# Optimization experiments

Measured on AMD Instinct MI355X. Metric: run time of the kernel, lower is better.

Reference implementation:

```python
import jax, jax.numpy as jnp
import numpy as np

B, S, T, H, NH, NL = 16, 128, 64, 128, 8, 4
DH = H // NH
FF = 2 * H
SCALE = 1.0 / float(np.sqrt(DH))


def _ln(x, s, b):
    m = x.mean(-1, keepdims=True)
    v = ((x - m) ** 2).mean(-1, keepdims=True)
    return (x - m) * jax.lax.rsqrt(v + 1e-5) * s + b


def _block(x, mask, p):
    Wq, bq, Wk, bk, Wv, bv, Wo, bo, s1, c1, W1, d1, W2, d2, s2, c2 = p
    N, L, _ = x.shape
    q = (x @ Wq + bq).reshape(N, L, NH, DH)
    k = (x @ Wk + bk).reshape(N, L, NH, DH)
    v = (x @ Wv + bv).reshape(N, L, NH, DH)
    scores = jnp.einsum('nqhd,nkhd->nhqk', q, k) * SCALE
    scores = jnp.where(mask[:, None, :, :], scores, -1e9)
    a = jax.nn.softmax(scores, axis=-1)
    o = jnp.einsum('nhqk,nkhd->nqhd', a, v).reshape(N, L, H)
    x = _ln(x + o @ Wo + bo, s1, c1)
    h = jax.nn.relu(x @ W1 + d1)
    return _ln(x + h @ W2 + d2, s2, c2)


def setup_inputs():
    key = jax.random.key(0)
    ks = jax.random.split(key, 16)
    g = lambda k, shape: jax.random.normal(k, shape, jnp.float32) * 0.02
    return {
        'polylines': jax.random.normal(ks[0], (B, S, T, H), jnp.float32),
        'lengths': jax.random.randint(ks[1], (B, S), 0, T + 1),
        'proj_w': g(ks[2], (H, H)), 'proj_b': jnp.zeros((H,), jnp.float32),
        'proj_ln_s': jnp.ones((H,), jnp.float32), 'proj_ln_b': jnp.zeros((H,), jnp.float32),
        'pos_emb': g(ks[3], (1, T, H)),
        'Wq': g(ks[4], (NL, H, H)), 'bq': jnp.zeros((NL, H), jnp.float32),
        'Wk': g(ks[5], (NL, H, H)), 'bk': jnp.zeros((NL, H), jnp.float32),
        'Wv': g(ks[6], (NL, H, H)), 'bv': jnp.zeros((NL, H), jnp.float32),
        'Wo': g(ks[7], (NL, H, H)), 'bo': jnp.zeros((NL, H), jnp.float32),
        'ln1_s': jnp.ones((NL, H), jnp.float32), 'ln1_b': jnp.zeros((NL, H), jnp.float32),
        'W1': g(ks[8], (NL, H, FF)), 'b1': jnp.zeros((NL, FF), jnp.float32),
        'W2': g(ks[9], (NL, FF, H)), 'b2': jnp.zeros((NL, H), jnp.float32),
        'ln2_s': jnp.ones((NL, H), jnp.float32), 'ln2_b': jnp.zeros((NL, H), jnp.float32),
    }


def reference(polylines, lengths, proj_w, proj_b, proj_ln_s, proj_ln_b, pos_emb,
              Wq, bq, Wk, bk, Wv, bv, Wo, bo, ln1_s, ln1_b, W1, b1, W2, b2, ln2_s, ln2_b):
    # valid[b,s,t] = t < lengths[b,s]; lengths==0 -> polyline absent (fully padded)
    valid = jnp.arange(T)[None, None, :] < lengths[:, :, None]  # [B,S,T]
    x = jnp.where(valid[..., None], polylines, -1.0)            # -1 pad as in np.pad(constant_values=-1)
    # mask_temporal[b,s] = outer(valid[b,s], valid[b,s])
    mask_t = (valid[:, :, :, None] & valid[:, :, None, :]).reshape(B * S, T, T)
    # mask_spatial[b,t] = outer(valid[b,:,t], valid[b,:,t])
    vs = jnp.transpose(valid, (0, 2, 1))                        # [B,T,S]
    mask_s = (vs[:, :, :, None] & vs[:, :, None, :]).reshape(B * T, S, S)

    x = x.reshape(B * S, T, H)
    x = jax.nn.relu(_ln(x @ proj_w + proj_b, proj_ln_s, proj_ln_b))  # MLP: Linear->LN->ReLU
    x = x + pos_emb[:, :T, :]

    mask = mask_t
    for i in range(NL):
        if i == NL // 2:
            # switch from temporal to spatial attention: [B*S,T,H] -> [B*T,S,H]
            x = x.reshape(B, S, T, H).transpose(0, 2, 1, 3).reshape(B * T, S, H)
            mask = mask_s
        p = (Wq[i], bq[i], Wk[i], bk[i], Wv[i], bv[i], Wo[i], bo[i],
             ln1_s[i], ln1_b[i], W1[i], b1[i], W2[i], b2[i], ln2_s[i], ln2_b[i])
        x = _block(x, mask, p)
    # faithful to original final reshape (treats [B*T,S,H] buffer as [B,S,T,H])
    return x.reshape(B, S, T, H)[:, 0, :]
```

## Files before the change

### kernel.cpp

```cpp
#include <hip/hip_runtime.h>

typedef short short8 __attribute__((ext_vector_type(8)));
typedef short short4_t __attribute__((ext_vector_type(4)));
typedef float floatx4 __attribute__((ext_vector_type(4)));
typedef unsigned short ushort_t;

#define B_ 16
#define S_ 128
#define T_ 64
#define H_ 128
#define FF_ 256
#define SCALEQK 0.25f

#define OFFP 0
#define OFFQ(l) (16384 + (l) * 65536)
#define OFFK(l) (OFFQ(l) + 16384)
#define OFFV(l) (OFFQ(l) + 32768)
#define OFFO(l) (OFFQ(l) + 49152)
#define OFFW1(l) (278528 + (l) * 65536)
#define OFFW2(l) (OFFW1(l) + 32768)

__device__ __forceinline__ float b2f(ushort_t u) {
    union { unsigned int i; float f; } x; x.i = ((unsigned int)u) << 16; return x.f;
}
__device__ __forceinline__ ushort_t f2b(float f) {
    union { float f; unsigned int i; } x; x.f = f;
    unsigned int r = x.i + 0x7fffu + ((x.i >> 16) & 1u);
    return (ushort_t)(r >> 16);
}
__device__ __forceinline__ int pack2b(float a, float b) {
    return (int)f2b(a) | ((int)f2b(b) << 16);
}

struct WtEnt { const float* src; int N; int K; int nclog2; int dstoff; };
struct WtArgs { WtEnt e[25]; };

__global__ __launch_bounds__(256) void wt_kernel(WtArgs a, ushort_t* __restrict__ dst) {
    WtEnt ent = a.e[blockIdx.x];
    const int tiles_c = ent.N >> 5;
    const int nt = (ent.K >> 5) * tiles_c;
    const int t = blockIdx.y;
    if (t >= nt) return;
    const int tc = t & (tiles_c - 1);
    const int tr = t >> ent.nclog2;
    __shared__ float ld[32 * 33];
    const int tid = threadIdx.x;
#pragma unroll
    for (int i = 0; i < 4; ++i) {
        int e = tid + i * 256;
        int rr = e >> 5, cc = e & 31;
        ld[rr * 33 + cc] = ent.src[(tr * 32 + rr) * ent.N + tc * 32 + cc];
    }
    __syncthreads();
    ushort_t* d = dst + ent.dstoff;
#pragma unroll
    for (int i = 0; i < 4; ++i) {
        int e = tid + i * 256;
        int rr = e >> 5, cc = e & 31;
        d[(tc * 32 + rr) * ent.K + tr * 32 + cc] = f2b(ld[cc * 33 + rr]);
    }
}

template<int RT, int CT, int KK>
__device__ __forceinline__ void mm_g(const ushort_t* aL, int sa,
                                     const ushort_t* __restrict__ wT,
                                     int colbase, int lane, floatx4 (&acc)[RT][CT]) {
    const int l15 = lane & 15, lq8 = (lane >> 4) * 8;
#pragma unroll
    for (int r = 0; r < RT; ++r)
#pragma unroll
        for (int c = 0; c < CT; ++c) acc[r][c] = (floatx4){0.f, 0.f, 0.f, 0.f};
#pragma unroll
    for (int k0 = 0; k0 < KK; k0 += 32) {
        short8 b[CT];
#pragma unroll
        for (int c = 0; c < CT; ++c)
            b[c] = *(const short8*)&wT[(colbase + c * 16 + l15) * KK + k0 + lq8];
#pragma unroll
        for (int r = 0; r < RT; ++r) {
            short8 a = *(const short8*)&aL[(r * 16 + l15) * sa + k0 + lq8];
#pragma unroll
            for (int c = 0; c < CT; ++c)
                acc[r][c] = __builtin_amdgcn_mfma_f32_16x16x32_bf16(a, b[c], acc[r][c], 0, 0, 0);
        }
    }
}

template<int RT, int CT>
__device__ __forceinline__ void add_bias(floatx4 (&acc)[RT][CT], const float* b,
                                         int colbase, int l15) {
#pragma unroll
    for (int c = 0; c < CT; ++c) {
        float bc = b[colbase + c * 16 + l15];
#pragma unroll
        for (int r = 0; r < RT; ++r)
#pragma unroll
            for (int g = 0; g < 4; ++g) acc[r][c][g] += bc;
    }
}

template<int RT, int CT>
__device__ __forceinline__ void add_resid_reg(floatx4 (&acc)[RT][CT],
                                              const float (&res)[RT][CT][4]) {
#pragma unroll
    for (int r = 0; r < RT; ++r)
#pragma unroll
        for (int c = 0; c < CT; ++c)
#pragma unroll
            for (int g = 0; g < 4; ++g) acc[r][c][g] += res[r][c][g];
}
template<int RT, int CT>
__device__ __forceinline__ void save_resid(float (&res)[RT][CT][4],
                                           const floatx4 (&acc)[RT][CT]) {
#pragma unroll
    for (int r = 0; r < RT; ++r)
#pragma unroll
        for (int c = 0; c < CT; ++c)
#pragma unroll
            for (int g = 0; g < 4; ++g) res[r][c][g] = acc[r][c][g];
}

template<int RT, int CT>
__device__ __forceinline__ void st_n(const floatx4 (&acc)[RT][CT], ushort_t* dst, int stride,
                                     int colbase, int l15, int lq) {
#pragma unroll
    for (int r = 0; r < RT; ++r)
#pragma unroll
        for (int g = 0; g < 4; ++g) {
            int row = r * 16 + lq * 4 + g;
#pragma unroll
            for (int c = 0; c < CT; ++c)
                dst[row * stride + colbase + c * 16 + l15] = f2b(acc[r][c][g]);
        }
}

template<int RT, int CT>
__device__ __forceinline__ void st_t(const floatx4 (&acc)[RT][CT], ushort_t* dst, int stride,
                                     int colbase, int l15, int lq) {
#pragma unroll
    for (int r = 0; r < RT; ++r)
#pragma unroll
        for (int c = 0; c < CT; ++c) {
            int d = colbase + c * 16 + l15;
            short4_t p;
#pragma unroll
            for (int g = 0; g < 4; ++g) p[g] = (short)f2b(acc[r][c][g]);
            *(short4_t*)&dst[d * stride + r * 16 + lq * 4] = p;
        }
}

template<int RT, int CT>
__device__ __forceinline__ void ln_norm(floatx4 (&acc)[RT][CT], float* redL,
                                        const float* lns, const float* lnb,
                                        int colbase, int l15, int lq, int wv) {
#pragma unroll
    for (int r = 0; r < RT; ++r)
#pragma unroll
        for (int g = 0; g < 4; ++g) {
            float s = 0.f, q = 0.f;
#pragma unroll
            for (int c = 0; c < CT; ++c) { float v = acc[r][c][g]; s += v; q += v * v; }
            s += __shfl_xor(s, 1); s += __shfl_xor(s, 2); s += __shfl_xor(s, 4); s += __shfl_xor(s, 8);
            q += __shfl_xor(q, 1); q += __shfl_xor(q, 2); q += __shfl_xor(q, 4); q += __shfl_xor(q, 8);
            if (l15 == 0) {
                int row = r * 16 + lq * 4 + g;
                redL[row * 8 + wv] = s;
                redL[row * 8 + 4 + wv] = q;
            }
        }
    __syncthreads();
#pragma unroll
    for (int r = 0; r < RT; ++r)
#pragma unroll
        for (int g = 0; g < 4; ++g) {
            int row = r * 16 + lq * 4 + g;
            float4 S = *(float4*)&redL[row * 8];
            float4 Q = *(float4*)&redL[row * 8 + 4];
            float mean = (S.x + S.y + S.z + S.w) * (1.f / 128.f);
            float var = (Q.x + Q.y + Q.z + Q.w) * (1.f / 128.f) - mean * mean;
            float rstd = rsqrtf(var + 1e-5f);
#pragma unroll
            for (int c = 0; c < CT; ++c) {
                int col = colbase + c * 16 + l15;
                acc[r][c][g] = (acc[r][c][g] - mean) * rstd * lns[col] + lnb[col];
            }
        }
}

template<int JT>
__device__ __forceinline__ void softmax_pack(floatx4 (&st)[JT], bool iv, unsigned jm,
                                             int (&px)[JT][2]) {
    float ev[JT][4];
    float mx = -3.0e38f;
#pragma unroll
    for (int jt = 0; jt < JT; ++jt)
#pragma unroll
        for (int g = 0; g < 4; ++g) {
            bool ok = iv && ((jm >> (jt * 4 + g)) & 1u);
            float s = ok ? st[jt][g] * SCALEQK : -1e9f;
            ev[jt][g] = s; mx = fmaxf(mx, s);
        }
    mx = fmaxf(mx, __shfl_xor(mx, 16)); mx = fmaxf(mx, __shfl_xor(mx, 32));
    float sum = 0.f;
#pragma unroll
    for (int jt = 0; jt < JT; ++jt)
#pragma unroll
        for (int g = 0; g < 4; ++g) { float e = __expf(ev[jt][g] - mx); ev[jt][g] = e; sum += e; }
    sum += __shfl_xor(sum, 16); sum += __shfl_xor(sum, 32);
    float inv = 1.f / sum;
#pragma unroll
    for (int jt = 0; jt < JT; ++jt) {
        px[jt][0] = pack2b(ev[jt][0] * inv, ev[jt][1] * inv);
        px[jt][1] = pack2b(ev[jt][2] * inv, ev[jt][3] * inv);
    }
}

__device__ __forceinline__ short8 pfrag(const int (*px)[2], int jc, int lq, int l15) {
    const int jA = (lq & 1) * 32 + l15;
    int a0 = __shfl(px[jc * 2][0], jA);
    int a1 = __shfl(px[jc * 2][1], jA);
    int a2 = __shfl(px[jc * 2][0], jA + 16);
    int a3 = __shfl(px[jc * 2][1], jA + 16);
    int b0 = __shfl(px[jc * 2 + 1][0], jA);
    int b1 = __shfl(px[jc * 2 + 1][1], jA);
    int b2 = __shfl(px[jc * 2 + 1][0], jA + 16);
    int b3 = __shfl(px[jc * 2 + 1][1], jA + 16);
    const bool t = (lq >> 1) != 0;
    union { int4 i; short8 s; } u;
    u.i = make_int4(t ? b0 : a0, t ? b1 : a1, t ? b2 : a2, t ? b3 : a3);
    return u.s;
}
__device__ __forceinline__ short8 vfrag(const ushort_t* vT, int stride, int row, int off) {
    int2 a = *(const int2*)&vT[row * stride + off];
    int2 b = *(const int2*)&vT[row * stride + off + 4];
    union { int4 i; short8 s; } u;
    u.i = make_int4(a.x, a.y, b.x, b.y);
    return u.s;
}

__global__ __launch_bounds__(256, 2) void k1_mega(
    const float* __restrict__ poly, const int* __restrict__ lens,
    const ushort_t* __restrict__ wt,
    const float* __restrict__ projb, const float* __restrict__ pls,
    const float* __restrict__ plb, const float* __restrict__ pos,
    const float* __restrict__ bq0, const float* __restrict__ bk0,
    const float* __restrict__ bv0, const float* __restrict__ bo0,
    const float* __restrict__ l1s0, const float* __restrict__ l1b0,
    const float* __restrict__ b10, const float* __restrict__ b20,
    const float* __restrict__ l2s0, const float* __restrict__ l2b0,
    const float* __restrict__ bq1, const float* __restrict__ bk1,
    const float* __restrict__ bv1,
    ushort_t* __restrict__ o1, float* __restrict__ xr0f)
{
    __shared__ ushort_t pool[34816];
    __shared__ float redL[512];
    __shared__ float psL[8 * 68];
    __shared__ float q1L[128];
    ushort_t* xL = pool;
    ushort_t* qL = pool + 8704;
    ushort_t* kL = pool + 17408;
    ushort_t* vT = pool + 26112;
    ushort_t* hL = pool + 17408;

    const int tid = threadIdx.x, lane = tid & 63, wv = tid >> 6;
    const int l15 = lane & 15, lq = lane >> 4;
    const int gid = blockIdx.x;
    const int len = lens[gid];

    {
        const float* pg = poly + (size_t)gid * 8192;
#pragma unroll
        for (int it = 0; it < 8; ++it) {
            int e4 = (tid + it * 256) * 4;
            int row = e4 >> 7, col = e4 & 127;
            float4 f = *(const float4*)(pg + e4);
            if (row >= len) { f.x = -1.f; f.y = -1.f; f.z = -1.f; f.w = -1.f; }
            short4_t u;
            u[0] = (short)f2b(f.x); u[1] = (short)f2b(f.y);
            u[2] = (short)f2b(f.z); u[3] = (short)f2b(f.w);
            *(short4_t*)&xL[row * 136 + col] = u;
        }
    }
    __syncthreads();

    floatx4 a2[4][2];
    float xre[4][2][4];

    mm_g<4, 2, 128>(xL, 136, wt + OFFP, wv * 32, lane, a2);
    add_bias<4, 2>(a2, projb, wv * 32, l15);
    ln_norm<4, 2>(a2, redL, pls, plb, wv * 32, l15, lq, wv);
    __syncthreads();
#pragma unroll
    for (int r = 0; r < 4; ++r)
#pragma unroll
        for (int gg = 0; gg < 4; ++gg) {
            int row = r * 16 + lq * 4 + gg;
#pragma unroll
            for (int c = 0; c < 2; ++c) {
                int col = wv * 32 + c * 16 + l15;
                float v = fmaxf(a2[r][c][gg], 0.f) + pos[row * 128 + col];
                xre[r][c][gg] = v;
                xL[row * 136 + col] = f2b(v);
            }
        }
    __syncthreads();

    mm_g<4, 2, 128>(xL, 136, wt + OFFQ(0), wv * 32, lane, a2);
    add_bias<4, 2>(a2, bq0, wv * 32, l15);
    st_n<4, 2>(a2, qL, 136, wv * 32, l15, lq);
    mm_g<4, 2, 128>(xL, 136, wt + OFFK(0), wv * 32, lane, a2);
    add_bias<4, 2>(a2, bk0, wv * 32, l15);
    st_n<4, 2>(a2, kL, 136, wv * 32, l15, lq);
    mm_g<4, 2, 128>(xL, 136, wt + OFFV(0), wv * 32, lane, a2);
    add_bias<4, 2>(a2, bv0, wv * 32, l15);
    st_t<4, 2>(a2, vT, 68, wv * 32, l15, lq);
    __syncthreads();

    {
        const int iRow = wv * 16 + l15;
        const bool iv = iRow < len;
        unsigned jm = 0;
#pragma unroll
        for (int jt = 0; jt < 4; ++jt)
#pragma unroll
            for (int gg = 0; gg < 4; ++gg)
                if (jt * 16 + lq * 4 + gg < len) jm |= (1u << (jt * 4 + gg));
        for (int h = 0; h < 8; ++h) {
            const int hc = h * 16;
            short8 z8 = {0, 0, 0, 0, 0, 0, 0, 0};
            short8 bqf = z8;
            if (lq < 2) bqf = *(const short8*)&qL[iRow * 136 + hc + lq * 8];
            floatx4 st[4];
#pragma unroll
            for (int jt = 0; jt < 4; ++jt) {
                short8 ak = z8;
                if (lq < 2) ak = *(const short8*)&kL[(jt * 16 + l15) * 136 + hc + lq * 8];
                floatx4 zz = {0.f, 0.f, 0.f, 0.f};
                st[jt] = __builtin_amdgcn_mfma_f32_16x16x32_bf16(ak, bqf, zz, 0, 0, 0);
            }
            int px[4][2];
            softmax_pack<4>(st, iv, jm, px);
            floatx4 ao = {0.f, 0.f, 0.f, 0.f};
#pragma unroll
            for (int jc = 0; jc < 2; ++jc) {
                short8 av = vfrag(vT, 68, hc + l15, jc * 32 + lq * 8);
                short8 bp = pfrag(px, jc, lq, l15);
                ao = __builtin_amdgcn_mfma_f32_16x16x32_bf16(av, bp, ao, 0, 0, 0);
            }
            short4_t w;
#pragma unroll
            for (int gg = 0; gg < 4; ++gg) w[gg] = (short)f2b(ao[gg]);
            *(short4_t*)&qL[iRow * 136 + hc + lq * 4] = w;
        }
    }
    __syncthreads();

    mm_g<4, 2, 128>(qL, 136, wt + OFFO(0), wv * 32, lane, a2);
    add_bias<4, 2>(a2, bo0, wv * 32, l15);
    add_resid_reg<4, 2>(a2, xre);
    ln_norm<4, 2>(a2, redL, l1s0, l1b0, wv * 32, l15, lq, wv);
    save_resid<4, 2>(xre, a2);
    st_n<4, 2>(a2, xL, 136, wv * 32, l15, lq);
    __syncthreads();

    {
        floatx4 a4[4][4];
        mm_g<4, 4, 128>(xL, 136, wt + OFFW1(0), wv * 64, lane, a4);
        add_bias<4, 4>(a4, b10, wv * 64, l15);
#pragma unroll
        for (int r = 0; r < 4; ++r)
#pragma unroll
            for (int c = 0; c < 4; ++c)
#pragma unroll
                for (int gg = 0; gg < 4; ++gg) a4[r][c][gg] = fmaxf(a4[r][c][gg], 0.f);
        st_n<4, 4>(a4, hL, 272, wv * 64, l15, lq);
    }
    __syncthreads();

    mm_g<4, 2, 256>(hL, 272, wt + OFFW2(0), wv * 32, lane, a2);
    add_bias<4, 2>(a2, b20, wv * 32, l15);
    add_resid_reg<4, 2>(a2, xre);
    ln_norm<4, 2>(a2, redL, l2s0, l2b0, wv * 32, l15, lq, wv);
    save_resid<4, 2>(xre, a2);
    st_n<4, 2>(a2, xL, 136, wv * 32, l15, lq);
    if (lq == 0) {
#pragma unroll
        for (int c = 0; c < 2; ++c)
            xr0f[(size_t)gid * 128 + wv * 32 + c * 16 + l15] = a2[0][c][0];
    }
    __syncthreads();

    mm_g<4, 2, 128>(xL, 136, wt + OFFK(1), wv * 32, lane, a2);
    add_bias<4, 2>(a2, bk1, wv * 32, l15);
    st_n<4, 2>(a2, kL, 136, wv * 32, l15, lq);
    mm_g<4, 2, 128>(xL, 136, wt + OFFV(1), wv * 32, lane, a2);
    add_bias<4, 2>(a2, bv1, wv * 32, l15);
    st_t<4, 2>(a2, vT, 68, wv * 32, l15, lq);
    if (tid < 128) {
        int d = tid;
        float a = bq1[d];
        const ushort_t* wq = wt + OFFQ(1) + d * 128;
#pragma unroll 4
        for (int j0 = 0; j0 < 128; j0 += 8) {
            short8 w8 = *(const short8*)&wq[j0];
            short8 x8 = *(const short8*)&xL[j0];
#pragma unroll
            for (int q = 0; q < 8; ++q)
                a = fmaf(b2f((ushort_t)x8[q]), b2f((ushort_t)w8[q]), a);
        }
        q1L[d] = a;
    }
    __syncthreads();

    {
        int h = tid >> 5, jj = tid & 31;
        int hc = h * 16;
        float s[2];
#pragma unroll
        for (int half = 0; half < 2; ++half) {
            int j = jj + half * 32;
            float a = 0.f;
            short8 k0v = *(const short8*)&kL[j * 136 + hc];
            short8 k1v = *(const short8*)&kL[j * 136 + hc + 8];
#pragma unroll
            for (int q = 0; q < 8; ++q) {
                a = fmaf(q1L[hc + q], b2f((ushort_t)k0v[q]), a);
                a = fmaf(q1L[hc + 8 + q], b2f((ushort_t)k1v[q]), a);
            }
            s[half] = (j < len) ? a * SCALEQK : -1e9f;
        }
        float mx = fmaxf(s[0], s[1]);
#pragma unroll
        for (int d = 1; d < 32; d <<= 1) mx = fmaxf(mx, __shfl_xor(mx, d));
        float e0 = __expf(s[0] - mx), e1 = __expf(s[1] - mx);
        float sum = e0 + e1;
#pragma unroll
        for (int d = 1; d < 32; d <<= 1) sum += __shfl_xor(sum, d);
        float inv = 1.f / sum;
        psL[h * 68 + jj] = e0 * inv;
        psL[h * 68 + jj + 32] = e1 * inv;
    }
    __syncthreads();
    if (tid < 128) {
        int h = tid >> 4, d = tid & 15, hc = h * 16;
        float a = 0.f;
#pragma unroll 4
        for (int j0 = 0; j0 < 64; j0 += 4) {
            float4 p4 = *(const float4*)&psL[h * 68 + j0];
            short4_t v4 = *(const short4_t*)&vT[(hc + d) * 68 + j0];
            a += p4.x * b2f((ushort_t)v4[0]) + p4.y * b2f((ushort_t)v4[1])
               + p4.z * b2f((ushort_t)v4[2]) + p4.w * b2f((ushort_t)v4[3]);
        }
        o1[(size_t)gid * 128 + hc + d] = f2b(a);
    }
}

__global__ __launch_bounds__(256, 1) void k2_mega(
    const ushort_t* __restrict__ o1, const float* __restrict__ xr0f,
    const int* __restrict__ lens, const ushort_t* __restrict__ wt,
    const float* __restrict__ bq, const float* __restrict__ bk,
    const float* __restrict__ bv, const float* __restrict__ bo,
    const float* __restrict__ l1s, const float* __restrict__ l1b,
    const float* __restrict__ b1, const float* __restrict__ b2,
    const float* __restrict__ l2s, const float* __restrict__ l2b,
    float* __restrict__ outp)
{
    __shared__ ushort_t pool[69632];
    __shared__ float redL[1024];
    __shared__ int vldL[128];
    ushort_t* xL = pool;
    ushort_t* qL = pool + 17408;
    ushort_t* kL = pool + 34816;
    ushort_t* vT = pool + 52224;
    ushort_t* hL = pool + 34816;

    const int tid = threadIdx.x, lane = tid & 63, wv = tid >> 6;
    const int l15 = lane & 15, lq = lane >> 4;
    const int b = blockIdx.x;
    const size_t rowg = (size_t)b * 128;

#pragma unroll
    for (int it = 0; it < 8; ++it) {
        int e8 = tid + it * 256;
        int row = e8 >> 4, kg = e8 & 15;
        *(short8*)&xL[row * 136 + kg * 8] = *(const short8*)&o1[(rowg + row) * 128 + kg * 8];
    }
    if (tid < 128) vldL[tid] = (lens[b * 128 + tid] > 0) ? 1 : 0;
    __syncthreads();

    unsigned jm = 0;
#pragma unroll
    for (int jt = 0; jt < 8; ++jt)
#pragma unroll
        for (int g = 0; g < 4; ++g)
            if (vldL[jt * 16 + lq * 4 + g]) jm |= (1u << (jt * 4 + g));

    float xre[8][2][4];
#pragma unroll
    for (int r = 0; r < 8; ++r)
#pragma unroll
        for (int c = 0; c < 2; ++c)
#pragma unroll
            for (int g = 0; g < 4; ++g)
                xre[r][c][g] = xr0f[(rowg + r * 16 + lq * 4 + g) * 128 + wv * 32 + c * 16 + l15];

    floatx4 a2[8][2];

    for (int l = 1; l < 4; ++l) {
        if (l >= 2) {
            mm_g<8, 2, 128>(xL, 136, wt + OFFQ(l), wv * 32, lane, a2);
            add_bias<8, 2>(a2, bq + l * H_, wv * 32, l15);
            st_n<8, 2>(a2, qL, 136, wv * 32, l15, lq);
            mm_g<8, 2, 128>(xL, 136, wt + OFFK(l), wv * 32, lane, a2);
            add_bias<8, 2>(a2, bk + l * H_, wv * 32, l15);
            st_n<8, 2>(a2, kL, 136, wv * 32, l15, lq);
            mm_g<8, 2, 128>(xL, 136, wt + OFFV(l), wv * 32, lane, a2);
            add_bias<8, 2>(a2, bv + l * H_, wv * 32, l15);
            st_t<8, 2>(a2, vT, 136, wv * 32, l15, lq);
            __syncthreads();
            for (int h = 0; h < 8; ++h) {
                const int hc = h * 16;
#pragma unroll
                for (int iblk = 0; iblk < 2; ++iblk) {
                    const int iRow = iblk * 64 + wv * 16 + l15;
                    const bool iv = vldL[iRow] != 0;
                    short8 z8 = {0, 0, 0, 0, 0, 0, 0, 0};
                    short8 bqf = z8;
                    if (lq < 2) bqf = *(const short8*)&qL[iRow * 136 + hc + lq * 8];
                    floatx4 st[8];
#pragma unroll
                    for (int jt = 0; jt < 8; ++jt) {
                        short8 ak = z8;
                        if (lq < 2) ak = *(const short8*)&kL[(jt * 16 + l15) * 136 + hc + lq * 8];
                        floatx4 zz = {0.f, 0.f, 0.f, 0.f};
                        st[jt] = __builtin_amdgcn_mfma_f32_16x16x32_bf16(ak, bqf, zz, 0, 0, 0);
                    }
                    int px[8][2];
                    softmax_pack<8>(st, iv, jm, px);
                    floatx4 ao = {0.f, 0.f, 0.f, 0.f};
#pragma unroll
                    for (int jc = 0; jc < 4; ++jc) {
                        short8 av = vfrag(vT, 136, hc + l15, jc * 32 + lq * 8);
                        short8 bp = pfrag(px, jc, lq, l15);
                        ao = __builtin_amdgcn_mfma_f32_16x16x32_bf16(av, bp, ao, 0, 0, 0);
                    }
                    short4_t w;
#pragma unroll
                    for (int g = 0; g < 4; ++g) w[g] = (short)f2b(ao[g]);
                    *(short4_t*)&qL[iRow * 136 + hc + lq * 4] = w;
                }
            }
            __syncthreads();
        }

        const ushort_t* aIn = (l == 1) ? xL : qL;
        mm_g<8, 2, 128>(aIn, 136, wt + OFFO(l), wv * 32, lane, a2);
        add_bias<8, 2>(a2, bo + l * H_, wv * 32, l15);
        add_resid_reg<8, 2>(a2, xre);
        ln_norm<8, 2>(a2, redL, l1s + l * H_, l1b + l * H_, wv * 32, l15, lq, wv);
        save_resid<8, 2>(xre, a2);
        st_n<8, 2>(a2, xL, 136, wv * 32, l15, lq);
        __syncthreads();

        {
            floatx4 a4[8][4];
            mm_g<8, 4, 128>(xL, 136, wt + OFFW1(l), wv * 64, lane, a4);
            add_bias<8, 4>(a4, b1 + l * FF_, wv * 64, l15);
#pragma unroll
            for (int r = 0; r < 8; ++r)
#pragma unroll
                for (int c = 0; c < 4; ++c)
#pragma unroll
                    for (int g = 0; g < 4; ++g) a4[r][c][g] = fmaxf(a4[r][c][g], 0.f);
            st_n<8, 4>(a4, hL, 272, wv * 64, l15, lq);
        }
        __syncthreads();

        mm_g<8, 2, 256>(hL, 272, wt + OFFW2(l), wv * 32, lane, a2);
        add_bias<8, 2>(a2, b2 + l * H_, wv * 32, l15);
        add_resid_reg<8, 2>(a2, xre);
        ln_norm<8, 2>(a2, redL, l2s + l * H_, l2b + l * H_, wv * 32, l15, lq, wv);
        if (l == 3) {
#pragma unroll
            for (int r = 0; r < 4; ++r)
#pragma unroll
                for (int c = 0; c < 2; ++c)
#pragma unroll
                    for (int g = 0; g < 4; ++g) {
                        int row = r * 16 + lq * 4 + g;
                        outp[((size_t)(b * 64 + row)) * 128 + wv * 32 + c * 16 + l15] = a2[r][c][g];
                    }
        } else {
            save_resid<8, 2>(xre, a2);
            st_n<8, 2>(a2, xL, 136, wv * 32, l15, lq);
            __syncthreads();
        }
    }
}

extern "C" void kernel_launch(void* const* d_in, const int* in_sizes, int n_in,
                              void* d_out, int out_size, void* d_ws, size_t ws_size,
                              hipStream_t stream)
{
    const float* poly   = (const float*)d_in[0];
    const int*   lens   = (const int*)d_in[1];
    const float* proj_w = (const float*)d_in[2];
    const float* proj_b = (const float*)d_in[3];
    const float* pls    = (const float*)d_in[4];
    const float* plb    = (const float*)d_in[5];
    const float* pos    = (const float*)d_in[6];
    const float* Wq = (const float*)d_in[7];
    const float* bq = (const float*)d_in[8];
    const float* Wk = (const float*)d_in[9];
    const float* bk = (const float*)d_in[10];
    const float* Wv = (const float*)d_in[11];
    const float* bv = (const float*)d_in[12];
    const float* Wo = (const float*)d_in[13];
    const float* bo = (const float*)d_in[14];
    const float* l1s = (const float*)d_in[15];
    const float* l1b = (const float*)d_in[16];
    const float* W1 = (const float*)d_in[17];
    const float* b1 = (const float*)d_in[18];
    const float* W2 = (const float*)d_in[19];
    const float* b2 = (const float*)d_in[20];
    const float* l2s = (const float*)d_in[21];
    const float* l2b = (const float*)d_in[22];
    float* outp = (float*)d_out;

    char* base = (char*)d_ws;
    ushort_t* wt    = (ushort_t*)base;
    ushort_t* o1buf = (ushort_t*)(base + 1081344);
    float* xr0f     = (float*)(base + 1605632);

    const int HH = H_ * H_, HF = H_ * FF_;
    WtArgs wa;
    wa.e[0] = {proj_w, 128, 128, 2, OFFP};
    for (int l = 0; l < 4; ++l) {
        wa.e[1 + l * 4 + 0] = {Wq + l * HH, 128, 128, 2, OFFQ(l)};
        wa.e[1 + l * 4 + 1] = {Wk + l * HH, 128, 128, 2, OFFK(l)};
        wa.e[1 + l * 4 + 2] = {Wv + l * HH, 128, 128, 2, OFFV(l)};
        wa.e[1 + l * 4 + 3] = {Wo + l * HH, 128, 128, 2, OFFO(l)};
    }
    for (int l = 0; l < 4; ++l) {
        wa.e[17 + l * 2 + 0] = {W1 + l * HF, 256, 128, 3, OFFW1(l)};
        wa.e[17 + l * 2 + 1] = {W2 + l * HF, 128, 256, 2, OFFW2(l)};
    }
    wt_kernel<<<dim3(25, 32), 256, 0, stream>>>(wa, wt);

    k1_mega<<<dim3(2048), 256, 0, stream>>>(
        poly, lens, wt,
        proj_b, pls, plb, pos,
        bq, bk, bv, bo, l1s, l1b, b1, b2, l2s, l2b,
        bq + H_, bk + H_, bv + H_,
        o1buf, xr0f);

    k2_mega<<<dim3(16), 256, 0, stream>>>(
        o1buf, xr0f, lens, wt,
        bq, bk, bv, bo, l1s, l1b, b1, b2, l2s, l2b,
        outp);
}
```

Baseline: 474.6 us.

## Widen spatial-stage k2_mega blocks to 1024 threads with 2D wave tiling

The second mega-kernel runs only 16 blocks, so each block is now given 16 waves instead of 4. Waves are split into row groups and column groups for the GEMMs, and into head × row-half pairs for attention. A new layer-norm variant reduces partial sums across column waves within each row group. The goal is more latency hiding and more parallel work per CU on a badly under-occupied grid. In exchange there are more barriers, a smaller per-wave register tile, and a tighter register budget per thread.

Result: no change. 468.9 us (-1.2%).

```diff
diff --git a/kernel.cpp b/kernel.cpp
--- a/kernel.cpp
+++ b/kernel.cpp
@@ -174,6 +174,44 @@
 #pragma unroll
         for (int g = 0; g < 4; ++g) {
             int row = r * 16 + lq * 4 + g;
+            float4 S = *(float4*)&redL[row * 8];
+            float4 Q = *(float4*)&redL[row * 8 + 4];
+            float mean = (S.x + S.y + S.z + S.w) * (1.f / 128.f);
+            float var = (Q.x + Q.y + Q.z + Q.w) * (1.f / 128.f) - mean * mean;
+            float rstd = rsqrtf(var + 1e-5f);
+#pragma unroll
+            for (int c = 0; c < CT; ++c) {
+                int col = colbase + c * 16 + l15;
+                acc[r][c][g] = (acc[r][c][g] - mean) * rstd * lns[col] + lnb[col];
+            }
+        }
+}
+
+template<int RT, int CT>
+__device__ __forceinline__ void ln_normW(floatx4 (&acc)[RT][CT], float* redL,
+                                         const float* lns, const float* lnb,
+                                         int colbase, int rowbase, int l15, int lq, int wc) {
+#pragma unroll
+    for (int r = 0; r < RT; ++r)
+#pragma unroll
+        for (int g = 0; g < 4; ++g) {
+            float s = 0.f, q = 0.f;
+#pragma unroll
+            for (int c = 0; c < CT; ++c) { float v = acc[r][c][g]; s += v; q += v * v; }
+            s += __shfl_xor(s, 1); s += __shfl_xor(s, 2); s += __shfl_xor(s, 4); s += __shfl_xor(s, 8);
+            q += __shfl_xor(q, 1); q += __shfl_xor(q, 2); q += __shfl_xor(q, 4); q += __shfl_xor(q, 8);
+            if (l15 == 0) {
+                int row = rowbase + r * 16 + lq * 4 + g;
+                redL[row * 8 + wc] = s;
+                redL[row * 8 + 4 + wc] = q;
+            }
+        }
+    __syncthreads();
+#pragma unroll
+    for (int r = 0; r < RT; ++r)
+#pragma unroll
+        for (int g = 0; g < 4; ++g) {
+            int row = rowbase + r * 16 + lq * 4 + g;
             float4 S = *(float4*)&redL[row * 8];
             float4 Q = *(float4*)&redL[row * 8 + 4];
             float mean = (S.x + S.y + S.z + S.w) * (1.f / 128.f);
@@ -455,7 +493,7 @@
     }
 }
 
-__global__ __launch_bounds__(256, 1) void k2_mega(
+__global__ __launch_bounds__(1024, 1) void k2_mega(
     const ushort_t* __restrict__ o1, const float* __restrict__ xr0f,
     const int* __restrict__ lens, const ushort_t* __restrict__ wt,
     const float* __restrict__ bq, const float* __restrict__ bk,
@@ -476,12 +514,14 @@
 
     const int tid = threadIdx.x, lane = tid & 63, wv = tid >> 6;
     const int l15 = lane & 15, lq = lane >> 4;
+    const int wc = wv & 3, wr = wv >> 2;
+    const int cb2 = wc * 32, cb4 = wc * 64, rb = wr * 32;
     const int b = blockIdx.x;
     const size_t rowg = (size_t)b * 128;
 
 #pragma unroll
-    for (int it = 0; it < 8; ++it) {
-        int e8 = tid + it * 256;
+    for (int it = 0; it < 2; ++it) {
+        int e8 = tid + it * 1024;
         int row = e8 >> 4, kg = e8 & 15;
         *(short8*)&xL[row * 136 + kg * 8] = *(const short8*)&o1[(rowg + row) * 128 + kg * 8];
     }
@@ -495,34 +535,33 @@
         for (int g = 0; g < 4; ++g)
             if (vldL[jt * 16 + lq * 4 + g]) jm |= (1u << (jt * 4 + g));
 
-    float xre[8][2][4];
-#pragma unroll
-    for (int r = 0; r < 8; ++r)
+    float xre[2][2][4];
+#pragma unroll
+    for (int r = 0; r < 2; ++r)
 #pragma unroll
         for (int c = 0; c < 2; ++c)
 #pragma unroll
             for (int g = 0; g < 4; ++g)
-                xre[r][c][g] = xr0f[(rowg + r * 16 + lq * 4 + g) * 128 + wv * 32 + c * 16 + l15];
-
-    floatx4 a2[8][2];
+                xre[r][c][g] = xr0f[(rowg + rb + r * 16 + lq * 4 + g) * 128 + cb2 + c * 16 + l15];
+
+    floatx4 a2[2][2];
 
     for (int l = 1; l < 4; ++l) {
         if (l >= 2) {
-            mm_g<8, 2, 128>(xL, 136, wt + OFFQ(l), wv * 32, lane, a2);
-            add_bias<8, 2>(a2, bq + l * H_, wv * 32, l15);
-            st_n<8, 2>(a2, qL, 136, wv * 32, l15, lq);
-            mm_g<8, 2, 128>(xL, 136, wt + OFFK(l), wv * 32, lane, a2);
-            add_bias<8, 2>(a2, bk + l * H_, wv * 32, l15);
-            st_n<8, 2>(a2, kL, 136, wv * 32, l15, lq);
-            mm_g<8, 2, 128>(xL, 136, wt + OFFV(l), wv * 32, lane, a2);
-            add_bias<8, 2>(a2, bv + l * H_, wv * 32, l15);
-            st_t<8, 2>(a2, vT, 136, wv * 32, l15, lq);
+            mm_g<2, 2, 128>(xL + rb * 136, 136, wt + OFFQ(l), cb2, lane, a2);
+            add_bias<2, 2>(a2, bq + l * H_, cb2, l15);
+            st_n<2, 2>(a2, qL + rb * 136, 136, cb2, l15, lq);
+            mm_g<2, 2, 128>(xL + rb * 136, 136, wt + OFFK(l), cb2, lane, a2);
+            add_bias<2, 2>(a2, bk + l * H_, cb2, l15);
+            st_n<2, 2>(a2, kL + rb * 136, 136, cb2, l15, lq);
+            mm_g<2, 2, 128>(xL + rb * 136, 136, wt + OFFV(l), cb2, lane, a2);
+            add_bias<2, 2>(a2, bv + l * H_, cb2, l15);
+            st_t<2, 2>(a2, vT + rb, 136, cb2, l15, lq);
             __syncthreads();
-            for (int h = 0; h < 8; ++h) {
-                const int hc = h * 16;
-#pragma unroll
-                for (int iblk = 0; iblk < 2; ++iblk) {
-                    const int iRow = iblk * 64 + wv * 16 + l15;
+            {
+                const int h = wv & 7, hc = h * 16, ihalf = wv >> 3;
+                for (int u = 0; u < 4; ++u) {
+                    const int iRow = ihalf * 64 + u * 16 + l15;
                     const bool iv = vldL[iRow] != 0;
                     short8 z8 = {0, 0, 0, 0, 0, 0, 0, 0};
                     short8 bqf = z8;
@@ -553,46 +592,48 @@
             __syncthreads();
         }
 
-        const ushort_t* aIn = (l == 1) ? xL : qL;
-        mm_g<8, 2, 128>(aIn, 136, wt + OFFO(l), wv * 32, lane, a2);
-        add_bias<8, 2>(a2, bo + l * H_, wv * 32, l15);
-        add_resid_reg<8, 2>(a2, xre);
-        ln_norm<8, 2>(a2, redL, l1s + l * H_, l1b + l * H_, wv * 32, l15, lq, wv);
-        save_resid<8, 2>(xre, a2);
-        st_n<8, 2>(a2, xL, 136, wv * 32, l15, lq);
+        const ushort_t* aIn = ((l == 1) ? xL : qL) + rb * 136;
+        mm_g<2, 2, 128>(aIn, 136, wt + OFFO(l), cb2, lane, a2);
+        add_bias<2, 2>(a2, bo + l * H_, cb2, l15);
+        add_resid_reg<2, 2>(a2, xre);
+        ln_normW<2, 2>(a2, redL, l1s + l * H_, l1b + l * H_, cb2, rb, l15, lq, wc);
+        save_resid<2, 2>(xre, a2);
+        st_n<2, 2>(a2, xL + rb * 136, 136, cb2, l15, lq);
         __syncthreads();
 
         {
-            floatx4 a4[8][4];
-            mm_g<8, 4, 128>(xL, 136, wt + OFFW1(l), wv * 64, lane, a4);
-            add_bias<8, 4>(a4, b1 + l * FF_, wv * 64, l15);
-#pragma unroll
-            for (int r = 0; r < 8; ++r)
+            floatx4 a4[2][4];
+            mm_g<2, 4, 128>(xL + rb * 136, 136, wt + OFFW1(l), cb4, lane, a4);
+            add_bias<2, 4>(a4, b1 + l * FF_, cb4, l15);
+#pragma unroll
+            for (int r = 0; r < 2; ++r)
 #pragma unroll
                 for (int c = 0; c < 4; ++c)
 #pragma unroll
                     for (int g = 0; g < 4; ++g) a4[r][c][g] = fmaxf(a4[r][c][g], 0.f);
-            st_n<8, 4>(a4, hL, 272, wv * 64, l15, lq);
+            st_n<2, 4>(a4, hL + rb * 272, 272, cb4, l15, lq);
         }
         __syncthreads();
 
-        mm_g<8, 2, 256>(hL, 272, wt + OFFW2(l), wv * 32, lane, a2);
-        add_bias<8, 2>(a2, b2 + l * H_, wv * 32, l15);
-        add_resid_reg<8, 2>(a2, xre);
-        ln_norm<8, 2>(a2, redL, l2s + l * H_, l2b + l * H_, wv * 32, l15, lq, wv);
+        mm_g<2, 2, 256>(hL + rb * 272, 272, wt + OFFW2(l), cb2, lane, a2);
+        add_bias<2, 2>(a2, b2 + l * H_, cb2, l15);
+        add_resid_reg<2, 2>(a2, xre);
+        ln_normW<2, 2>(a2, redL, l2s + l * H_, l2b + l * H_, cb2, rb, l15, lq, wc);
         if (l == 3) {
-#pragma unroll
-            for (int r = 0; r < 4; ++r)
-#pragma unroll
-                for (int c = 0; c < 2; ++c)
-#pragma unroll
-                    for (int g = 0; g < 4; ++g) {
-                        int row = r * 16 + lq * 4 + g;
-                        outp[((size_t)(b * 64 + row)) * 128 + wv * 32 + c * 16 + l15] = a2[r][c][g];
-                    }
+            if (wr < 2) {
+#pragma unroll
+                for (int r = 0; r < 2; ++r)
+#pragma unroll
+                    for (int c = 0; c < 2; ++c)
+#pragma unroll
+                        for (int g = 0; g < 4; ++g) {
+                            int row = rb + r * 16 + lq * 4 + g;
+                            outp[((size_t)(b * 64 + row)) * 128 + cb2 + c * 16 + l15] = a2[r][c][g];
+                        }
+            }
         } else {
-            save_resid<8, 2>(xre, a2);
-            st_n<8, 2>(a2, xL, 136, wv * 32, l15, lq);
+            save_resid<2, 2>(xre, a2);
+            st_n<2, 2>(a2, xL + rb * 136, 136, cb2, l15, lq);
             __syncthreads();
         }
     }
@@ -654,7 +695,7 @@
         bq + H_, bk + H_, bv + H_,
         o1buf, xr0f);
 
-    k2_mega<<<dim3(16), 256, 0, stream>>>(
+    k2_mega<<<dim3(16), 1024, 0, stream>>>(
         o1buf, xr0f, lens, wt,
         bq, bk, bv, bo, l1s, l1b, b1, b2, l2s, l2b,
         outp);
```

## Split spatial-stage megakernel into per-head attention and row-tiled FFN kernels

Applied to the files above, without the earlier changes.

The single 16-block k2_mega kernel that ran layers 1-3 is replaced by a chain of launches. k2a handles attention per (group, head) on a 16x8 grid, and k2b handles the output projection, LayerNorms and FFN on 64-row tiles across 32 blocks. The aim is to spread the work across many more CUs than the 16 the megakernel used. The cost is extra launches and global round trips of activations and the fp32 residual between kernels, and each head block recomputes nothing but reloads the full x tile. The final k2b uses 16 blocks and only writes the first 64 rows per group, matching the earlier final output.

New measurement: 385.5 us. 1.23x faster.

```diff
diff --git a/kernel.cpp b/kernel.cpp
--- a/kernel.cpp
+++ b/kernel.cpp
@@ -455,146 +455,170 @@
     }
 }
 
-__global__ __launch_bounds__(256, 1) void k2_mega(
-    const ushort_t* __restrict__ o1, const float* __restrict__ xr0f,
-    const int* __restrict__ lens, const ushort_t* __restrict__ wt,
+__global__ __launch_bounds__(256, 3) void k2a(
+    const ushort_t* __restrict__ xg, const int* __restrict__ lens,
+    const ushort_t* __restrict__ wt, int l,
     const float* __restrict__ bq, const float* __restrict__ bk,
-    const float* __restrict__ bv, const float* __restrict__ bo,
-    const float* __restrict__ l1s, const float* __restrict__ l1b,
-    const float* __restrict__ b1, const float* __restrict__ b2,
-    const float* __restrict__ l2s, const float* __restrict__ l2b,
-    float* __restrict__ outp)
+    const float* __restrict__ bv,
+    ushort_t* __restrict__ aob)
 {
-    __shared__ ushort_t pool[69632];
-    __shared__ float redL[1024];
+    __shared__ ushort_t xL[128 * 136];
+    __shared__ ushort_t qL[128 * 24];
+    __shared__ ushort_t kL[128 * 24];
+    __shared__ ushort_t vT[16 * 136];
     __shared__ int vldL[128];
-    ushort_t* xL = pool;
-    ushort_t* qL = pool + 17408;
-    ushort_t* kL = pool + 34816;
-    ushort_t* vT = pool + 52224;
-    ushort_t* hL = pool + 34816;
 
     const int tid = threadIdx.x, lane = tid & 63, wv = tid >> 6;
     const int l15 = lane & 15, lq = lane >> 4;
-    const int b = blockIdx.x;
-    const size_t rowg = (size_t)b * 128;
+    const int g = blockIdx.x, h = blockIdx.y, hc = h * 16;
+    const size_t rowg = (size_t)g * 128;
 
 #pragma unroll
     for (int it = 0; it < 8; ++it) {
         int e8 = tid + it * 256;
         int row = e8 >> 4, kg = e8 & 15;
-        *(short8*)&xL[row * 136 + kg * 8] = *(const short8*)&o1[(rowg + row) * 128 + kg * 8];
-    }
-    if (tid < 128) vldL[tid] = (lens[b * 128 + tid] > 0) ? 1 : 0;
+        *(short8*)&xL[row * 136 + kg * 8] = *(const short8*)&xg[(rowg + row) * 128 + kg * 8];
+    }
+    if (tid < 128) vldL[tid] = (lens[g * 128 + tid] > 0) ? 1 : 0;
     __syncthreads();
 
     unsigned jm = 0;
 #pragma unroll
     for (int jt = 0; jt < 8; ++jt)
 #pragma unroll
-        for (int g = 0; g < 4; ++g)
-            if (vldL[jt * 16 + lq * 4 + g]) jm |= (1u << (jt * 4 + g));
-
-    float xre[8][2][4];
-#pragma unroll
-    for (int r = 0; r < 8; ++r)
+        for (int gg = 0; gg < 4; ++gg)
+            if (vldL[jt * 16 + lq * 4 + gg]) jm |= (1u << (jt * 4 + gg));
+
+    {
+        floatx4 a1[2][1];
+        mm_g<2, 1, 128>(xL + (wv * 32) * 136, 136, wt + OFFQ(l), hc, lane, a1);
+        add_bias<2, 1>(a1, bq, hc, l15);
+        st_n<2, 1>(a1, qL + (wv * 32) * 24, 24, 0, l15, lq);
+        mm_g<2, 1, 128>(xL + (wv * 32) * 136, 136, wt + OFFK(l), hc, lane, a1);
+        add_bias<2, 1>(a1, bk, hc, l15);
+        st_n<2, 1>(a1, kL + (wv * 32) * 24, 24, 0, l15, lq);
+        mm_g<2, 1, 128>(xL + (wv * 32) * 136, 136, wt + OFFV(l), hc, lane, a1);
+        add_bias<2, 1>(a1, bv, hc, l15);
+        st_t<2, 1>(a1, vT + wv * 32, 136, 0, l15, lq);
+    }
+    __syncthreads();
+
+    for (int u = 0; u < 2; ++u) {
+        const int iRow = wv * 32 + u * 16 + l15;
+        const bool iv = vldL[iRow] != 0;
+        short8 z8 = {0, 0, 0, 0, 0, 0, 0, 0};
+        short8 bqf = z8;
+        if (lq < 2) bqf = *(const short8*)&qL[iRow * 24 + lq * 8];
+        floatx4 st[8];
+#pragma unroll
+        for (int jt = 0; jt < 8; ++jt) {
+            short8 ak = z8;
+            if (lq < 2) ak = *(const short8*)&kL[(jt * 16 + l15) * 24 + lq * 8];
+            floatx4 zz = {0.f, 0.f, 0.f, 0.f};
+            st[jt] = __builtin_amdgcn_mfma_f32_16x16x32_bf16(ak, bqf, zz, 0, 0, 0);
+        }
+        int px[8][2];
+        softmax_pack<8>(st, iv, jm, px);
+        floatx4 ao = {0.f, 0.f, 0.f, 0.f};
+#pragma unroll
+        for (int jc = 0; jc < 4; ++jc) {
+            short8 av = vfrag(vT, 136, l15, jc * 32 + lq * 8);
+            short8 bp = pfrag(px, jc, lq, l15);
+            ao = __builtin_amdgcn_mfma_f32_16x16x32_bf16(av, bp, ao, 0, 0, 0);
+        }
+        short4_t w;
+#pragma unroll
+        for (int gg = 0; gg < 4; ++gg) w[gg] = (short)f2b(ao[gg]);
+        *(short4_t*)&aob[(rowg + iRow) * 128 + hc + lq * 4] = w;
+    }
+}
+
+template<bool FINAL>
+__global__ __launch_bounds__(256, 2) void k2b(
+    const ushort_t* __restrict__ ain, float* __restrict__ xr,
+    const ushort_t* __restrict__ wt, int l,
+    const float* __restrict__ bo_l, const float* __restrict__ l1s_l,
+    const float* __restrict__ l1b_l, const float* __restrict__ b1_l,
+    const float* __restrict__ b2_l, const float* __restrict__ l2s_l,
+    const float* __restrict__ l2b_l,
+    ushort_t* __restrict__ xg, float* __restrict__ outp)
+{
+    __shared__ ushort_t aL[64 * 136];
+    __shared__ ushort_t hL[64 * 272];
+    __shared__ float redL[512];
+
+    const int tid = threadIdx.x, lane = tid & 63, wv = tid >> 6;
+    const int l15 = lane & 15, lq = lane >> 4;
+    const size_t rowbase = (size_t)blockIdx.x * (FINAL ? 128 : 64);
+
+#pragma unroll
+    for (int it = 0; it < 4; ++it) {
+        int e8 = tid + it * 256;
+        int row = e8 >> 4, kg = e8 & 15;
+        *(short8*)&aL[row * 136 + kg * 8] = *(const short8*)&ain[(rowbase + row) * 128 + kg * 8];
+    }
+    __syncthreads();
+
+    floatx4 a2[4][2];
+    float xre[4][2][4];
+
+    mm_g<4, 2, 128>(aL, 136, wt + OFFO(l), wv * 32, lane, a2);
+    add_bias<4, 2>(a2, bo_l, wv * 32, l15);
+#pragma unroll
+    for (int r = 0; r < 4; ++r)
 #pragma unroll
         for (int c = 0; c < 2; ++c)
 #pragma unroll
-            for (int g = 0; g < 4; ++g)
-                xre[r][c][g] = xr0f[(rowg + r * 16 + lq * 4 + g) * 128 + wv * 32 + c * 16 + l15];
-
-    floatx4 a2[8][2];
-
-    for (int l = 1; l < 4; ++l) {
-        if (l >= 2) {
-            mm_g<8, 2, 128>(xL, 136, wt + OFFQ(l), wv * 32, lane, a2);
-            add_bias<8, 2>(a2, bq + l * H_, wv * 32, l15);
-            st_n<8, 2>(a2, qL, 136, wv * 32, l15, lq);
-            mm_g<8, 2, 128>(xL, 136, wt + OFFK(l), wv * 32, lane, a2);
-            add_bias<8, 2>(a2, bk + l * H_, wv * 32, l15);
-            st_n<8, 2>(a2, kL, 136, wv * 32, l15, lq);
-            mm_g<8, 2, 128>(xL, 136, wt + OFFV(l), wv * 32, lane, a2);
-            add_bias<8, 2>(a2, bv + l * H_, wv * 32, l15);
-            st_t<8, 2>(a2, vT, 136, wv * 32, l15, lq);
-            __syncthreads();
-            for (int h = 0; h < 8; ++h) {
-                const int hc = h * 16;
-#pragma unroll
-                for (int iblk = 0; iblk < 2; ++iblk) {
-                    const int iRow = iblk * 64 + wv * 16 + l15;
-                    const bool iv = vldL[iRow] != 0;
-                    short8 z8 = {0, 0, 0, 0, 0, 0, 0, 0};
-                    short8 bqf = z8;
-                    if (lq < 2) bqf = *(const short8*)&qL[iRow * 136 + hc + lq * 8];
-                    floatx4 st[8];
-#pragma unroll
-                    for (int jt = 0; jt < 8; ++jt) {
-                        short8 ak = z8;
-                        if (lq < 2) ak = *(const short8*)&kL[(jt * 16 + l15) * 136 + hc + lq * 8];
-                        floatx4 zz = {0.f, 0.f, 0.f, 0.f};
-                        st[jt] = __builtin_amdgcn_mfma_f32_16x16x32_bf16(ak, bqf, zz, 0, 0, 0);
-                    }
-                    int px[8][2];
-                    softmax_pack<8>(st, iv, jm, px);
-                    floatx4 ao = {0.f, 0.f, 0.f, 0.f};
-#pragma unroll
-                    for (int jc = 0; jc < 4; ++jc) {
-                        short8 av = vfrag(vT, 136, hc + l15, jc * 32 + lq * 8);
-                        short8 bp = pfrag(px, jc, lq, l15);
-                        ao = __builtin_amdgcn_mfma_f32_16x16x32_bf16(av, bp, ao, 0, 0, 0);
-                    }
-                    short4_t w;
-#pragma unroll
-                    for (int g = 0; g < 4; ++g) w[g] = (short)f2b(ao[g]);
-                    *(short4_t*)&qL[iRow * 136 + hc + lq * 4] = w;
+            for (int gg = 0; gg < 4; ++gg)
+                a2[r][c][gg] += xr[(rowbase + r * 16 + lq * 4 + gg) * 128 + wv * 32 + c * 16 + l15];
+    ln_norm<4, 2>(a2, redL, l1s_l, l1b_l, wv * 32, l15, lq, wv);
+    save_resid<4, 2>(xre, a2);
+    st_n<4, 2>(a2, aL, 136, wv * 32, l15, lq);
+    __syncthreads();
+
+    {
+        floatx4 a4[4][4];
+        mm_g<4, 4, 128>(aL, 136, wt + OFFW1(l), wv * 64, lane, a4);
+        add_bias<4, 4>(a4, b1_l, wv * 64, l15);
+#pragma unroll
+        for (int r = 0; r < 4; ++r)
+#pragma unroll
+            for (int c = 0; c < 4; ++c)
+#pragma unroll
+                for (int gg = 0; gg < 4; ++gg) a4[r][c][gg] = fmaxf(a4[r][c][gg], 0.f);
+        st_n<4, 4>(a4, hL, 272, wv * 64, l15, lq);
+    }
+    __syncthreads();
+
+    mm_g<4, 2, 256>(hL, 272, wt + OFFW2(l), wv * 32, lane, a2);
+    add_bias<4, 2>(a2, b2_l, wv * 32, l15);
+    add_resid_reg<4, 2>(a2, xre);
+    ln_norm<4, 2>(a2, redL, l2s_l, l2b_l, wv * 32, l15, lq, wv);
+
+    if (FINAL) {
+#pragma unroll
+        for (int r = 0; r < 4; ++r)
+#pragma unroll
+            for (int c = 0; c < 2; ++c)
+#pragma unroll
+                for (int gg = 0; gg < 4; ++gg) {
+                    int row = r * 16 + lq * 4 + gg;
+                    outp[((size_t)(blockIdx.x * 64 + row)) * 128 + wv * 32 + c * 16 + l15] =
+                        a2[r][c][gg];
                 }
-            }
-            __syncthreads();
-        }
-
-        const ushort_t* aIn = (l == 1) ? xL : qL;
-        mm_g<8, 2, 128>(aIn, 136, wt + OFFO(l), wv * 32, lane, a2);
-        add_bias<8, 2>(a2, bo + l * H_, wv * 32, l15);
-        add_resid_reg<8, 2>(a2, xre);
-        ln_norm<8, 2>(a2, redL, l1s + l * H_, l1b + l * H_, wv * 32, l15, lq, wv);
-        save_resid<8, 2>(xre, a2);
-        st_n<8, 2>(a2, xL, 136, wv * 32, l15, lq);
-        __syncthreads();
-
-        {
-            floatx4 a4[8][4];
-            mm_g<8, 4, 128>(xL, 136, wt + OFFW1(l), wv * 64, lane, a4);
-            add_bias<8, 4>(a4, b1 + l * FF_, wv * 64, l15);
-#pragma unroll
-            for (int r = 0; r < 8; ++r)
-#pragma unroll
-                for (int c = 0; c < 4; ++c)
-#pragma unroll
-                    for (int g = 0; g < 4; ++g) a4[r][c][g] = fmaxf(a4[r][c][g], 0.f);
-            st_n<8, 4>(a4, hL, 272, wv * 64, l15, lq);
-        }
-        __syncthreads();
-
-        mm_g<8, 2, 256>(hL, 272, wt + OFFW2(l), wv * 32, lane, a2);
-        add_bias<8, 2>(a2, b2 + l * H_, wv * 32, l15);
-        add_resid_reg<8, 2>(a2, xre);
-        ln_norm<8, 2>(a2, redL, l2s + l * H_, l2b + l * H_, wv * 32, l15, lq, wv);
-        if (l == 3) {
-#pragma unroll
-            for (int r = 0; r < 4; ++r)
-#pragma unroll
-                for (int c = 0; c < 2; ++c)
-#pragma unroll
-                    for (int g = 0; g < 4; ++g) {
-                        int row = r * 16 + lq * 4 + g;
-                        outp[((size_t)(b * 64 + row)) * 128 + wv * 32 + c * 16 + l15] = a2[r][c][g];
-                    }
-        } else {
-            save_resid<8, 2>(xre, a2);
-            st_n<8, 2>(a2, xL, 136, wv * 32, l15, lq);
-            __syncthreads();
-        }
+    } else {
+#pragma unroll
+        for (int r = 0; r < 4; ++r)
+#pragma unroll
+            for (int c = 0; c < 2; ++c)
+#pragma unroll
+                for (int gg = 0; gg < 4; ++gg) {
+                    size_t grow = rowbase + r * 16 + lq * 4 + gg;
+                    int col = wv * 32 + c * 16 + l15;
+                    float v = a2[r][c][gg];
+                    xg[grow * 128 + col] = f2b(v);
+                    xr[grow * 128 + col] = v;
+                }
     }
 }
 
@@ -631,6 +655,8 @@
     ushort_t* wt    = (ushort_t*)base;
     ushort_t* o1buf = (ushort_t*)(base + 1081344);
     float* xr0f     = (float*)(base + 1605632);
+    ushort_t* xgbuf = (ushort_t*)(base + 2654208);
+    ushort_t* aob   = (ushort_t*)(base + 3178496);
 
     const int HH = H_ * H_, HF = H_ * FF_;
     WtArgs wa;
@@ -654,8 +680,22 @@
         bq + H_, bk + H_, bv + H_,
         o1buf, xr0f);
 
-    k2_mega<<<dim3(16), 256, 0, stream>>>(
-        o1buf, xr0f, lens, wt,
-        bq, bk, bv, bo, l1s, l1b, b1, b2, l2s, l2b,
-        outp);
-}
+    k2b<false><<<dim3(32), 256, 0, stream>>>(
+        o1buf, xr0f, wt, 1,
+        bo + H_, l1s + H_, l1b + H_, b1 + FF_, b2 + H_, l2s + H_, l2b + H_,
+        xgbuf, nullptr);
+    k2a<<<dim3(16, 8), 256, 0, stream>>>(
+        xgbuf, lens, wt, 2, bq + 2 * H_, bk + 2 * H_, bv + 2 * H_, aob);
+    k2b<false><<<dim3(32), 256, 0, stream>>>(
+        aob, xr0f, wt, 2,
+        bo + 2 * H_, l1s + 2 * H_, l1b + 2 * H_, b1 + 2 * FF_, b2 + 2 * H_,
+        l2s + 2 * H_, l2b + 2 * H_,
+        xgbuf, nullptr);
+    k2a<<<dim3(16, 8), 256, 0, stream>>>(
+        xgbuf, lens, wt, 3, bq + 3 * H_, bk + 3 * H_, bv + 3 * H_, aob);
+    k2b<true><<<dim3(16), 256, 0, stream>>>(
+        aob, xr0f, wt, 3,
+        bo + 3 * H_, l1s + 3 * H_, l1b + 3 * H_, b1 + 3 * FF_, b2 + 3 * H_,
+        l2s + 3 * H_, l2b + 3 * H_,
+        nullptr, outp);
+}
```
